# Kernel optimization log

Measured on AMD Instinct MI355X. Metric: run time of the kernel, lower is better.

Reference implementation:

```python
import jax, jax.numpy as jnp
import numpy as np

B, H, W, C = 8, 224, 224, 96
WS, SS, NH = 7, 3, 3  # window size, shift size, num heads
HD = C // NH
N = WS * WS
nW = (H // WS) * (W // WS)


def _rel_pos_index():
    coords = np.stack(np.meshgrid(np.arange(WS), np.arange(WS), indexing='ij'))  # (2,WS,WS)
    flat = coords.reshape(2, -1)
    rel = (flat[:, :, None] - flat[:, None, :]).transpose(1, 2, 0)  # (N,N,2)
    rel[:, :, 0] += WS - 1
    rel[:, :, 1] += WS - 1
    rel[:, :, 0] *= 2 * WS - 1
    return jnp.asarray(rel.sum(-1))  # (N,N) int


def _shift_mask():
    img = np.zeros((H, W), np.int32)
    cnt = 0
    sls = (slice(0, -WS), slice(-WS, -SS), slice(-SS, None))
    for hs in sls:
        for ws_ in sls:
            img[hs, ws_] = cnt
            cnt += 1
    m = img.reshape(H // WS, WS, W // WS, WS).transpose(0, 2, 1, 3).reshape(-1, N)  # (nW,N)
    diff = m[:, :, None] - m[:, None, :]
    return jnp.asarray(np.where(diff != 0, -100.0, 0.0).astype(np.float32))  # (nW,N,N)


def setup_inputs() -> dict:
    key = jax.random.key(0)
    ks = jax.random.split(key, 10)
    s = 0.02
    return {
        'x': jax.random.normal(ks[0], (B, H * W, C), jnp.float32),
        'mask': _shift_mask(),
        'norm1_g': jnp.ones((C,), jnp.float32),
        'norm1_b': jnp.zeros((C,), jnp.float32),
        'qkv_w': s * jax.random.normal(ks[1], (3 * C, C), jnp.float32),
        'qkv_b': jnp.zeros((3 * C,), jnp.float32),
        'rpb_table': s * jax.random.normal(ks[2], ((2 * WS - 1) * (2 * WS - 1), NH), jnp.float32),
        'proj_w': s * jax.random.normal(ks[3], (C, C), jnp.float32),
        'proj_b': jnp.zeros((C,), jnp.float32),
        'norm2_g': jnp.ones((C,), jnp.float32),
        'norm2_b': jnp.zeros((C,), jnp.float32),
        'fc1_w': s * jax.random.normal(ks[4], (4 * C, C), jnp.float32),
        'fc1_b': jnp.zeros((4 * C,), jnp.float32),
        'fc2_w': s * jax.random.normal(ks[5], (C, 4 * C), jnp.float32),
        'fc2_b': jnp.zeros((C,), jnp.float32),
    }


def _ln(x, g, b):
    mu = x.mean(-1, keepdims=True)
    var = x.var(-1, keepdims=True)
    return (x - mu) * jax.lax.rsqrt(var + 1e-5) * g + b


def _win_partition(x):  # (B,H,W,C) -> (B*nW, N, C)
    x = x.reshape(B, H // WS, WS, W // WS, WS, C)
    return x.transpose(0, 1, 3, 2, 4, 5).reshape(-1, N, C)


def _win_reverse(w):  # (B*nW, N, C) -> (B,H,W,C)
    w = w.reshape(B, H // WS, W // WS, WS, WS, C)
    return w.transpose(0, 1, 3, 2, 4, 5).reshape(B, H, W, C)


def reference(x, mask, norm1_g, norm1_b, qkv_w, qkv_b, rpb_table, proj_w, proj_b,
              norm2_g, norm2_b, fc1_w, fc1_b, fc2_w, fc2_b):
    rel_idx = _rel_pos_index()  # (N,N) constant
    shortcut = x
    h = _ln(x, norm1_g, norm1_b).reshape(B, H, W, C)
    h = jnp.roll(h, shift=(-SS, -SS), axis=(1, 2))  # cyclic shift
    xw = _win_partition(h)  # (B*nW, N, C)
    B_ = xw.shape[0]
    qkv = (xw @ qkv_w.T + qkv_b).reshape(B_, N, 3, NH, HD).transpose(2, 0, 3, 1, 4)
    q, k, v = qkv[0], qkv[1], qkv[2]  # (B_,NH,N,HD)
    scale = HD ** -0.5
    attn = jnp.einsum('bhid,bhjd->bhij', q * scale, k)  # (B_,NH,N,N)
    bias = rpb_table[rel_idx.reshape(-1)].reshape(N, N, NH).transpose(2, 0, 1)  # (NH,N,N)
    attn = attn + bias[None]
    attn = attn.reshape(B, nW, NH, N, N) + mask[None, :, None]
    attn = jax.nn.softmax(attn.reshape(B_, NH, N, N), axis=-1)
    out = jnp.einsum('bhij,bhjd->bhid', attn, v).transpose(0, 2, 1, 3).reshape(B_, N, C)
    out = out @ proj_w.T + proj_b
    h = _win_reverse(out)
    h = jnp.roll(h, shift=(SS, SS), axis=(1, 2)).reshape(B, H * W, C)
    x = shortcut + h
    # MLP
    m = _ln(x, norm2_g, norm2_b)
    m = jax.nn.gelu(m @ fc1_w.T + fc1_b, approximate=False)
    m = m @ fc2_w.T + fc2_b
    return x + m
```

## Files before the change

### kernel.cpp

```cpp
#include <hip/hip_runtime.h>
#include <hip/hip_bf16.h>
#include <stdint.h>

typedef __attribute__((ext_vector_type(4))) float f32x4;
typedef __bf16 bfv8 __attribute__((ext_vector_type(8)));
typedef unsigned short u16x8 __attribute__((ext_vector_type(8)));

#define DEV static __device__ __forceinline__

DEV float b2f(unsigned short h) {
    unsigned u = ((unsigned)h) << 16;
    return __builtin_bit_cast(float, u);
}
DEV unsigned short f2b(float f) {
    unsigned u = __builtin_bit_cast(unsigned, f);
    u += 0x7fffu + ((u >> 16) & 1u);
    return (unsigned short)(u >> 16);
}
DEV unsigned short f2bn(float f) {
    return __builtin_bit_cast(unsigned short, (__bf16)f);
}
DEV bfv8 ldb8(const unsigned short* p) {
    return __builtin_bit_cast(bfv8, *(const u16x8*)p);
}

static constexpr int T = 401408;

__global__ __launch_bounds__(256) void k_prep(const float* __restrict__ qkvw,
                                              const float* __restrict__ projw,
                                              const float* __restrict__ w1,
                                              const float* __restrict__ w2,
                                              const float* __restrict__ rpb,
                                              const float* __restrict__ mask,
                                              unsigned short* __restrict__ wb,
                                              float* __restrict__ cmb) {
    int i = blockIdx.x * 256 + threadIdx.x;
    if (i < 110592) {
        float v;
        if (i < 27648) v = qkvw[i];
        else if (i < 36864) v = projw[i - 27648];
        else if (i < 73728) v = w1[i - 36864];
        else v = w2[i - 73728];
        wb[i] = f2b(v);
    } else if (i < 110592 + 49152) {
        int j = i - 110592;
        int t = j / 12288, rem = j - t * 12288;
        int h = rem >> 12, nm = rem & 4095;
        int n = nm >> 6, m = nm & 63;
        float v = -10000.f;
        if (n < 49 && m < 49) {
            int i1 = n / 7, j1 = n - i1 * 7, i2 = m / 7, j2 = m - i2 * 7;
            int rel = (i1 - i2 + 6) * 13 + (j1 - j2 + 6);
            int rep = ((t & 1) ? 31 : 0) + ((t & 2) ? 992 : 0);
            v = rpb[rel * 3 + h] + mask[rep * 2401 + n * 49 + m];
        }
        cmb[j] = v;
    }
}

__global__ __launch_bounds__(192) void k_attnf(const float* __restrict__ x,
                                               const float* __restrict__ g1,
                                               const float* __restrict__ be1,
                                               const unsigned short* __restrict__ qkvwb,
                                               const float* __restrict__ qkvb,
                                               const float* __restrict__ cmb,
                                               unsigned short* __restrict__ aout) {
    __shared__ unsigned short smem[10368 + 3 * 5120];
    unsigned short* xs = smem;

    unsigned win = blockIdx.x;
    unsigned b = win >> 10, widx = win & 1023u;
    unsigned wi = widx >> 5, wj = widx & 31u;
    int tid = threadIdx.x, wv = tid >> 6, lane = tid & 63;
    int half = lane >> 5, lch = lane & 31;

    for (int it = 0; it < 9; ++it) {
        int tok = it * 6 + wv * 2 + half;
        if (tok < 49) {
            unsigned i = (unsigned)tok / 7u, j = (unsigned)tok - i * 7u;
            unsigned sr = wi * 7 + i + 3; if (sr >= 224) sr -= 224;
            unsigned sc = wj * 7 + j + 3; if (sc >= 224) sc -= 224;
            const float* src = x + (size_t)(b * 50176u + sr * 224u + sc) * 96;
            float v0 = src[lch], v1 = src[lch + 32], v2 = src[lch + 64];
            float s = v0 + v1 + v2, q = v0 * v0 + v1 * v1 + v2 * v2;
#pragma unroll
            for (int off = 1; off < 32; off <<= 1) {
                s += __shfl_xor(s, off);
                q += __shfl_xor(q, off);
            }
            float mu = s * (1.f / 96.f);
            float rstd = rsqrtf(q * (1.f / 96.f) - mu * mu + 1e-5f);
            xs[tok * 104 + lch]      = f2bn((v0 - mu) * rstd * g1[lch] + be1[lch]);
            xs[tok * 104 + lch + 32] = f2bn((v1 - mu) * rstd * g1[lch + 32] + be1[lch + 32]);
            xs[tok * 104 + lch + 64] = f2bn((v2 - mu) * rstd * g1[lch + 64] + be1[lch + 64]);
        }
    }
    for (int t = tid; t < 15 * 96; t += 192)
        xs[(49 + t / 96) * 104 + (t % 96)] = 0;
    __syncthreads();

    int h = wv;
    int rlo = lane & 15, g4 = lane >> 4;
    bfv8 a[4][3];
#pragma unroll
    for (int mt = 0; mt < 4; ++mt)
#pragma unroll
        for (int ks = 0; ks < 3; ++ks)
            a[mt][ks] = ldb8(xs + (mt * 16 + rlo) * 104 + ks * 32 + g4 * 8);
    __syncthreads();

    unsigned short* vtH = smem + h * 3456;
    unsigned short* qH  = smem + 10368 + h * 5120;
    unsigned short* kH  = qH + 2560;
    unsigned short* pH  = qH;

    const float SC = 0.17677669529663687f;
    int colbase[6] = {32 * h, 32 * h + 16, 96 + 32 * h, 96 + 32 * h + 16,
                      192 + 32 * h, 192 + 32 * h + 16};
#pragma unroll
    for (int grp = 0; grp < 2; ++grp) {
        bfv8 wS[3][3];
        float bS[3];
#pragma unroll
        for (int q3 = 0; q3 < 3; ++q3) {
            int c = colbase[grp * 3 + q3] + rlo;
            wS[q3][0] = ldb8(qkvwb + (size_t)c * 96 + g4 * 8);
            wS[q3][1] = ldb8(qkvwb + (size_t)c * 96 + 32 + g4 * 8);
            wS[q3][2] = ldb8(qkvwb + (size_t)c * 96 + 64 + g4 * 8);
            bS[q3] = qkvb[c];
        }
#pragma unroll
        for (int q3 = 0; q3 < 3; ++q3) {
            int nt = grp * 3 + q3;
#pragma unroll
            for (int mt = 0; mt < 4; ++mt) {
                f32x4 acc = {0.f, 0.f, 0.f, 0.f};
                acc = __builtin_amdgcn_mfma_f32_16x16x32_bf16(a[mt][0], wS[q3][0], acc, 0, 0, 0);
                acc = __builtin_amdgcn_mfma_f32_16x16x32_bf16(a[mt][1], wS[q3][1], acc, 0, 0, 0);
                acc = __builtin_amdgcn_mfma_f32_16x16x32_bf16(a[mt][2], wS[q3][2], acc, 0, 0, 0);
#pragma unroll
                for (int r = 0; r < 4; ++r) {
                    int row = mt * 16 + g4 * 4 + r;
                    float v = acc[r] + bS[q3];
                    if (nt < 2) qH[row * 40 + nt * 16 + rlo] = f2bn(v * SC);
                    else if (nt < 4) kH[row * 40 + (nt - 2) * 16 + rlo] = f2bn(v);
                    else vtH[((nt - 4) * 16 + rlo) * 72 + row] = f2bn(v);
                }
            }
        }
    }
    vtH[32 * 72 + lane] = 0x3F80;

    bfv8 qf[4], kf[4];
#pragma unroll
    for (int t = 0; t < 4; ++t) {
        qf[t] = ldb8(qH + (t * 16 + rlo) * 40 + g4 * 8);
        kf[t] = ldb8(kH + (t * 16 + rlo) * 40 + g4 * 8);
    }
    f32x4 s[4][4];
#pragma unroll
    for (int mt = 0; mt < 4; ++mt)
#pragma unroll
        for (int nt = 0; nt < 4; ++nt) {
            f32x4 acc0 = {0.f, 0.f, 0.f, 0.f};
            s[mt][nt] = __builtin_amdgcn_mfma_f32_16x16x32_bf16(qf[mt], kf[nt], acc0, 0, 0, 0);
        }
    int type = ((wi == 31) ? 2 : 0) | ((wj == 31) ? 1 : 0);
    const float* crow = cmb + ((size_t)(type * 3 + h) << 12);
#pragma unroll
    for (int mt = 0; mt < 4; ++mt) {
#pragma unroll
        for (int r = 0; r < 4; ++r) {
            int n = mt * 16 + g4 * 4 + r;
            const float* cr = crow + n * 64;
#pragma unroll
            for (int nt = 0; nt < 4; ++nt) {
                int m = nt * 16 + rlo;
                pH[n * 72 + m] = f2bn(__expf(s[mt][nt][r] + cr[m]));
            }
        }
    }
    bfv8 vf[2][3];
#pragma unroll
    for (int ks = 0; ks < 2; ++ks)
#pragma unroll
        for (int db = 0; db < 3; ++db)
            vf[ks][db] = ldb8(vtH + (db * 16 + rlo) * 72 + ks * 32 + g4 * 8);
#pragma unroll
    for (int mt = 0; mt < 4; ++mt) {
        bfv8 pa0 = ldb8(pH + (mt * 16 + rlo) * 72 + g4 * 8);
        bfv8 pa1 = ldb8(pH + (mt * 16 + rlo) * 72 + 32 + g4 * 8);
        f32x4 acc[3];
#pragma unroll
        for (int db = 0; db < 3; ++db) {
            acc[db] = {0.f, 0.f, 0.f, 0.f};
            acc[db] = __builtin_amdgcn_mfma_f32_16x16x32_bf16(pa0, vf[0][db], acc[db], 0, 0, 0);
            acc[db] = __builtin_amdgcn_mfma_f32_16x16x32_bf16(pa1, vf[1][db], acc[db], 0, 0, 0);
        }
        float inv[4];
#pragma unroll
        for (int r = 0; r < 4; ++r)
            inv[r] = 1.f / __shfl(acc[2][r], lane & 48);
#pragma unroll
        for (int db = 0; db < 2; ++db) {
#pragma unroll
            for (int r = 0; r < 4; ++r) {
                int n = mt * 16 + g4 * 4 + r;
                if (n < 49)
                    aout[((size_t)win * 49 + n) * 96 + h * 32 + db * 16 + rlo] =
                        f2bn(acc[db][r] * inv[r]);
            }
        }
    }
}

__global__ __launch_bounds__(256, 4) void k_pm(const unsigned short* __restrict__ aout,
                                               const unsigned short* __restrict__ projwb,
                                               const float* __restrict__ projb,
                                               const float* __restrict__ x,
                                               const float* __restrict__ g2,
                                               const float* __restrict__ be2,
                                               const unsigned short* __restrict__ w1b,
                                               const float* __restrict__ bias1,
                                               const unsigned short* __restrict__ w2b,
                                               const float* __restrict__ bias2,
                                               float* __restrict__ out) {
    __shared__ unsigned short smem[64 * 204];
    unsigned short* xn  = smem;
    unsigned short* m1t = smem;

    int lane = threadIdx.x & 63, wv = threadIdx.x >> 6;
    int rlo = lane & 15, g4 = lane >> 4;
    size_t tok0 = (size_t)blockIdx.x * 64;
    size_t rowW = tok0 + wv * 16;

    bfv8 a0[3];
    {
        const unsigned short* p = aout + (rowW + rlo) * 96 + g4 * 8;
        a0[0] = ldb8(p); a0[1] = ldb8(p + 32); a0[2] = ldb8(p + 64);
    }
    int pix[4];
#pragma unroll
    for (int r = 0; r < 4; ++r) {
        unsigned wt = (unsigned)(rowW + g4 * 4 + r);
        unsigned win = wt / 49u, n = wt - win * 49u;
        unsigned b = win >> 10, widx = win & 1023u;
        unsigned wi = widx >> 5, wj = widx & 31u;
        unsigned i = n / 7u, j = n - i * 7u;
        unsigned sr = wi * 7 + i + 3; if (sr >= 224) sr -= 224;
        unsigned sc = wj * 7 + j + 3; if (sc >= 224) sc -= 224;
        pix[r] = (int)(b * 50176u + sr * 224u + sc);
    }

    float xv[6][4];
    float rs_[4] = {0.f, 0.f, 0.f, 0.f}, rq_[4] = {0.f, 0.f, 0.f, 0.f};
    for (int nt = 0; nt < 6; ++nt) {
        int c = nt * 16 + rlo;
        bfv8 b0 = ldb8(projwb + (size_t)c * 96 + g4 * 8);
        bfv8 b1 = ldb8(projwb + (size_t)c * 96 + 32 + g4 * 8);
        bfv8 b2 = ldb8(projwb + (size_t)c * 96 + 64 + g4 * 8);
        float bv = projb[c];
        f32x4 acc = {0.f, 0.f, 0.f, 0.f};
        acc = __builtin_amdgcn_mfma_f32_16x16x32_bf16(a0[0], b0, acc, 0, 0, 0);
        acc = __builtin_amdgcn_mfma_f32_16x16x32_bf16(a0[1], b1, acc, 0, 0, 0);
        acc = __builtin_amdgcn_mfma_f32_16x16x32_bf16(a0[2], b2, acc, 0, 0, 0);
#pragma unroll
        for (int r = 0; r < 4; ++r) {
            float v = acc[r] + bv + x[(size_t)pix[r] * 96 + c];
            xv[nt][r] = v;
            rs_[r] += v;
            rq_[r] += v * v;
        }
    }
    float mu[4], rstd[4];
#pragma unroll
    for (int r = 0; r < 4; ++r) {
        float s = rs_[r], q = rq_[r];
#pragma unroll
        for (int off = 1; off < 16; off <<= 1) {
            s += __shfl_xor(s, off);
            q += __shfl_xor(q, off);
        }
        mu[r] = s * (1.f / 96.f);
        rstd[r] = rsqrtf(q * (1.f / 96.f) - mu[r] * mu[r] + 1e-5f);
    }
#pragma unroll
    for (int nt = 0; nt < 6; ++nt) {
        int c = nt * 16 + rlo;
        float gg = g2[c], bb = be2[c];
#pragma unroll
        for (int r = 0; r < 4; ++r) {
            int row = wv * 16 + g4 * 4 + r;
            xn[row * 104 + c] = f2bn((xv[nt][r] - mu[r]) * rstd[r] * gg + bb);
        }
    }
    __syncthreads();

    bfv8 a[4][3];
#pragma unroll
    for (int mt = 0; mt < 4; ++mt)
#pragma unroll
        for (int ks = 0; ks < 3; ++ks)
            a[mt][ks] = ldb8(xn + (mt * 16 + rlo) * 104 + ks * 32 + g4 * 8);
    __syncthreads();

    f32x4 acc2[6];
#pragma unroll
    for (int nt = 0; nt < 6; ++nt) acc2[nt] = {0.f, 0.f, 0.f, 0.f};

#pragma unroll
    for (int half = 0; half < 2; ++half) {
#pragma unroll
        for (int nt = 0; nt < 3; ++nt) {
            int cl = wv * 48 + nt * 16 + rlo;
            int c = half * 192 + cl;
            bfv8 b0 = ldb8(w1b + (size_t)c * 96 + g4 * 8);
            bfv8 b1 = ldb8(w1b + (size_t)c * 96 + 32 + g4 * 8);
            bfv8 b2 = ldb8(w1b + (size_t)c * 96 + 64 + g4 * 8);
            float bv = bias1[c];
#pragma unroll
            for (int mt = 0; mt < 4; ++mt) {
                f32x4 acc = {0.f, 0.f, 0.f, 0.f};
                acc = __builtin_amdgcn_mfma_f32_16x16x32_bf16(a[mt][0], b0, acc, 0, 0, 0);
                acc = __builtin_amdgcn_mfma_f32_16x16x32_bf16(a[mt][1], b1, acc, 0, 0, 0);
                acc = __builtin_amdgcn_mfma_f32_16x16x32_bf16(a[mt][2], b2, acc, 0, 0, 0);
#pragma unroll
                for (int r = 0; r < 4; ++r) {
                    float v = acc[r] + bv;
                    float z = 1.5957691216057308f * (v + 0.044715f * v * v * v);
                    v = v / (1.f + __expf(-z));
                    m1t[(mt * 16 + g4 * 4 + r) * 204 + cl] = f2bn(v);
                }
            }
        }
        __syncthreads();
#pragma unroll
        for (int ks = 0; ks < 6; ++ks) {
            bfv8 am = ldb8(m1t + (wv * 16 + rlo) * 204 + ks * 32 + g4 * 8);
#pragma unroll
            for (int nt = 0; nt < 6; ++nt) {
                bfv8 bw = ldb8(w2b + (size_t)(nt * 16 + rlo) * 384 + half * 192 + ks * 32 + g4 * 8);
                acc2[nt] = __builtin_amdgcn_mfma_f32_16x16x32_bf16(am, bw, acc2[nt], 0, 0, 0);
            }
        }
        if (half == 0) __syncthreads();
    }

#pragma unroll
    for (int nt = 0; nt < 6; ++nt) {
        int c = nt * 16 + rlo;
        float bv = bias2[c];
#pragma unroll
        for (int r = 0; r < 4; ++r)
            out[(size_t)pix[r] * 96 + c] = acc2[nt][r] + bv + xv[nt][r];
    }
}

extern "C" void kernel_launch(void* const* d_in, const int* in_sizes, int n_in,
                              void* d_out, int out_size, void* d_ws, size_t ws_size,
                              hipStream_t stream) {
    const float* x     = (const float*)d_in[0];
    const float* mask  = (const float*)d_in[1];
    const float* n1g   = (const float*)d_in[2];
    const float* n1b   = (const float*)d_in[3];
    const float* qkvw  = (const float*)d_in[4];
    const float* qkvb  = (const float*)d_in[5];
    const float* rpb   = (const float*)d_in[6];
    const float* projw = (const float*)d_in[7];
    const float* projb = (const float*)d_in[8];
    const float* n2g   = (const float*)d_in[9];
    const float* n2b   = (const float*)d_in[10];
    const float* fc1w  = (const float*)d_in[11];
    const float* fc1b  = (const float*)d_in[12];
    const float* fc2w  = (const float*)d_in[13];
    const float* fc2b  = (const float*)d_in[14];

    if (ws_size < 77488128ULL) return;
    char* ws = (char*)d_ws;
    unsigned short* aout = (unsigned short*)ws;
    unsigned short* wb   = (unsigned short*)(ws + 77070336);
    float*          cmb  = (float*)(ws + 77291520);
    float*          out  = (float*)d_out;

    unsigned short* qkvwb  = wb;
    unsigned short* projwb = wb + 27648;
    unsigned short* fc1wb  = wb + 36864;
    unsigned short* fc2wb  = wb + 73728;

    k_prep<<<624, 256, 0, stream>>>(qkvw, projw, fc1w, fc2w, rpb, mask, wb, cmb);
    k_attnf<<<8192, 192, 0, stream>>>(x, n1g, n1b, qkvwb, qkvb, cmb, aout);
    k_pm<<<T / 64, 256, 0, stream>>>(aout, projwb, projb, x, n2g, n2b,
                                     fc1wb, fc1b, fc2wb, fc2b, out);
}
```

Before: 566.7 us.

## Swap MFMA operand order to get transposed outputs enabling vectorized stores and loads

Every MFMA call now passes operands in swapped order, so each lane holds four consecutive output columns for one row instead of four rows for one column. This allows packed 4-wide bf16 shared/global stores, float4 loads of bias, mask, x and LayerNorm params, and it cuts the LayerNorm reduction from 4x4 shuffles to 2 shuffles per stat. The pixel index is computed once per lane rather than four times. k_pm launch bounds also drop from 4 to 3 blocks per SM, giving more registers but lower occupancy, and the V-transposed store remains scattered.

Result: faster. 520.4 us (-8.2%).

```diff
diff --git a/kernel.cpp b/kernel.cpp
--- a/kernel.cpp
+++ b/kernel.cpp
@@ -5,6 +5,7 @@
 typedef __attribute__((ext_vector_type(4))) float f32x4;
 typedef __bf16 bfv8 __attribute__((ext_vector_type(8)));
 typedef unsigned short u16x8 __attribute__((ext_vector_type(8)));
+typedef unsigned short u16x4 __attribute__((ext_vector_type(4)));
 
 #define DEV static __device__ __forceinline__
 
@@ -22,6 +23,11 @@
 }
 DEV bfv8 ldb8(const unsigned short* p) {
     return __builtin_bit_cast(bfv8, *(const u16x8*)p);
+}
+DEV void stb4(unsigned short* p, f32x4 v) {
+    u16x4 o;
+    o[0] = f2bn(v[0]); o[1] = f2bn(v[1]); o[2] = f2bn(v[2]); o[3] = f2bn(v[3]);
+    *(u16x4*)p = o;
 }
 
 static constexpr int T = 401408;
@@ -120,14 +126,14 @@
 #pragma unroll
     for (int grp = 0; grp < 2; ++grp) {
         bfv8 wS[3][3];
-        float bS[3];
+        f32x4 bS[3];
 #pragma unroll
         for (int q3 = 0; q3 < 3; ++q3) {
             int c = colbase[grp * 3 + q3] + rlo;
             wS[q3][0] = ldb8(qkvwb + (size_t)c * 96 + g4 * 8);
             wS[q3][1] = ldb8(qkvwb + (size_t)c * 96 + 32 + g4 * 8);
             wS[q3][2] = ldb8(qkvwb + (size_t)c * 96 + 64 + g4 * 8);
-            bS[q3] = qkvb[c];
+            bS[q3] = *(const f32x4*)(qkvb + colbase[grp * 3 + q3] + g4 * 4);
         }
 #pragma unroll
         for (int q3 = 0; q3 < 3; ++q3) {
@@ -135,16 +141,21 @@
 #pragma unroll
             for (int mt = 0; mt < 4; ++mt) {
                 f32x4 acc = {0.f, 0.f, 0.f, 0.f};
-                acc = __builtin_amdgcn_mfma_f32_16x16x32_bf16(a[mt][0], wS[q3][0], acc, 0, 0, 0);
-                acc = __builtin_amdgcn_mfma_f32_16x16x32_bf16(a[mt][1], wS[q3][1], acc, 0, 0, 0);
-                acc = __builtin_amdgcn_mfma_f32_16x16x32_bf16(a[mt][2], wS[q3][2], acc, 0, 0, 0);
-#pragma unroll
-                for (int r = 0; r < 4; ++r) {
-                    int row = mt * 16 + g4 * 4 + r;
-                    float v = acc[r] + bS[q3];
-                    if (nt < 2) qH[row * 40 + nt * 16 + rlo] = f2bn(v * SC);
-                    else if (nt < 4) kH[row * 40 + (nt - 2) * 16 + rlo] = f2bn(v);
-                    else vtH[((nt - 4) * 16 + rlo) * 72 + row] = f2bn(v);
+                acc = __builtin_amdgcn_mfma_f32_16x16x32_bf16(wS[q3][0], a[mt][0], acc, 0, 0, 0);
+                acc = __builtin_amdgcn_mfma_f32_16x16x32_bf16(wS[q3][1], a[mt][1], acc, 0, 0, 0);
+                acc = __builtin_amdgcn_mfma_f32_16x16x32_bf16(wS[q3][2], a[mt][2], acc, 0, 0, 0);
+                int token = mt * 16 + rlo;
+                if (nt < 2) {
+                    f32x4 v = (acc + bS[q3]) * SC;
+                    stb4(qH + token * 40 + nt * 16 + g4 * 4, v);
+                } else if (nt < 4) {
+                    f32x4 v = acc + bS[q3];
+                    stb4(kH + token * 40 + (nt - 2) * 16 + g4 * 4, v);
+                } else {
+#pragma unroll
+                    for (int r = 0; r < 4; ++r)
+                        vtH[((nt - 4) * 16 + g4 * 4 + r) * 72 + token] =
+                            f2bn(acc[r] + bS[q3][r]);
                 }
             }
         }
@@ -163,21 +174,21 @@
 #pragma unroll
         for (int nt = 0; nt < 4; ++nt) {
             f32x4 acc0 = {0.f, 0.f, 0.f, 0.f};
-            s[mt][nt] = __builtin_amdgcn_mfma_f32_16x16x32_bf16(qf[mt], kf[nt], acc0, 0, 0, 0);
+            s[mt][nt] = __builtin_amdgcn_mfma_f32_16x16x32_bf16(kf[nt], qf[mt], acc0, 0, 0, 0);
         }
     int type = ((wi == 31) ? 2 : 0) | ((wj == 31) ? 1 : 0);
     const float* crow = cmb + ((size_t)(type * 3 + h) << 12);
 #pragma unroll
     for (int mt = 0; mt < 4; ++mt) {
-#pragma unroll
-        for (int r = 0; r < 4; ++r) {
-            int n = mt * 16 + g4 * 4 + r;
-            const float* cr = crow + n * 64;
-#pragma unroll
-            for (int nt = 0; nt < 4; ++nt) {
-                int m = nt * 16 + rlo;
-                pH[n * 72 + m] = f2bn(__expf(s[mt][nt][r] + cr[m]));
-            }
+        int query = mt * 16 + rlo;
+        const float* cr = crow + query * 64;
+#pragma unroll
+        for (int nt = 0; nt < 4; ++nt) {
+            f32x4 cv = *(const f32x4*)(cr + nt * 16 + g4 * 4);
+            f32x4 p;
+#pragma unroll
+            for (int r = 0; r < 4; ++r) p[r] = __expf(s[mt][nt][r] + cv[r]);
+            stb4(pH + query * 72 + nt * 16 + g4 * 4, p);
         }
     }
     bfv8 vf[2][3];
@@ -194,27 +205,23 @@
 #pragma unroll
         for (int db = 0; db < 3; ++db) {
             acc[db] = {0.f, 0.f, 0.f, 0.f};
-            acc[db] = __builtin_amdgcn_mfma_f32_16x16x32_bf16(pa0, vf[0][db], acc[db], 0, 0, 0);
-            acc[db] = __builtin_amdgcn_mfma_f32_16x16x32_bf16(pa1, vf[1][db], acc[db], 0, 0, 0);
-        }
-        float inv[4];
-#pragma unroll
-        for (int r = 0; r < 4; ++r)
-            inv[r] = 1.f / __shfl(acc[2][r], lane & 48);
-#pragma unroll
-        for (int db = 0; db < 2; ++db) {
-#pragma unroll
-            for (int r = 0; r < 4; ++r) {
-                int n = mt * 16 + g4 * 4 + r;
-                if (n < 49)
-                    aout[((size_t)win * 49 + n) * 96 + h * 32 + db * 16 + rlo] =
-                        f2bn(acc[db][r] * inv[r]);
-            }
-        }
-    }
-}
-
-__global__ __launch_bounds__(256, 4) void k_pm(const unsigned short* __restrict__ aout,
+            acc[db] = __builtin_amdgcn_mfma_f32_16x16x32_bf16(vf[0][db], pa0, acc[db], 0, 0, 0);
+            acc[db] = __builtin_amdgcn_mfma_f32_16x16x32_bf16(vf[1][db], pa1, acc[db], 0, 0, 0);
+        }
+        float inv = 1.f / __shfl(acc[2][0], rlo);
+        int query = mt * 16 + rlo;
+        if (query < 49) {
+            unsigned short* ob = aout + ((size_t)win * 49 + query) * 96 + h * 32;
+#pragma unroll
+            for (int db = 0; db < 2; ++db) {
+                f32x4 v = acc[db] * inv;
+                stb4(ob + db * 16 + g4 * 4, v);
+            }
+        }
+    }
+}
+
+__global__ __launch_bounds__(256, 3) void k_pm(const unsigned short* __restrict__ aout,
                                                const unsigned short* __restrict__ projwb,
                                                const float* __restrict__ projb,
                                                const float* __restrict__ x,
@@ -239,60 +246,54 @@
         const unsigned short* p = aout + (rowW + rlo) * 96 + g4 * 8;
         a0[0] = ldb8(p); a0[1] = ldb8(p + 32); a0[2] = ldb8(p + 64);
     }
-    int pix[4];
-#pragma unroll
-    for (int r = 0; r < 4; ++r) {
-        unsigned wt = (unsigned)(rowW + g4 * 4 + r);
+    int pix;
+    {
+        unsigned wt = (unsigned)(rowW + rlo);
         unsigned win = wt / 49u, n = wt - win * 49u;
         unsigned b = win >> 10, widx = win & 1023u;
         unsigned wi = widx >> 5, wj = widx & 31u;
         unsigned i = n / 7u, j = n - i * 7u;
         unsigned sr = wi * 7 + i + 3; if (sr >= 224) sr -= 224;
         unsigned sc = wj * 7 + j + 3; if (sc >= 224) sc -= 224;
-        pix[r] = (int)(b * 50176u + sr * 224u + sc);
-    }
-
-    float xv[6][4];
-    float rs_[4] = {0.f, 0.f, 0.f, 0.f}, rq_[4] = {0.f, 0.f, 0.f, 0.f};
+        pix = (int)(b * 50176u + sr * 224u + sc);
+    }
+    f32x4 xr4[6];
+#pragma unroll
+    for (int nt = 0; nt < 6; ++nt)
+        xr4[nt] = *(const f32x4*)(x + (size_t)pix * 96 + nt * 16 + g4 * 4);
+
+    f32x4 xv[6];
+    float rs = 0.f, rq = 0.f;
     for (int nt = 0; nt < 6; ++nt) {
         int c = nt * 16 + rlo;
         bfv8 b0 = ldb8(projwb + (size_t)c * 96 + g4 * 8);
         bfv8 b1 = ldb8(projwb + (size_t)c * 96 + 32 + g4 * 8);
         bfv8 b2 = ldb8(projwb + (size_t)c * 96 + 64 + g4 * 8);
-        float bv = projb[c];
+        f32x4 bv = *(const f32x4*)(projb + nt * 16 + g4 * 4);
         f32x4 acc = {0.f, 0.f, 0.f, 0.f};
-        acc = __builtin_amdgcn_mfma_f32_16x16x32_bf16(a0[0], b0, acc, 0, 0, 0);
-        acc = __builtin_amdgcn_mfma_f32_16x16x32_bf16(a0[1], b1, acc, 0, 0, 0);
-        acc = __builtin_amdgcn_mfma_f32_16x16x32_bf16(a0[2], b2, acc, 0, 0, 0);
+        acc = __builtin_amdgcn_mfma_f32_16x16x32_bf16(b0, a0[0], acc, 0, 0, 0);
+        acc = __builtin_amdgcn_mfma_f32_16x16x32_bf16(b1, a0[1], acc, 0, 0, 0);
+        acc = __builtin_amdgcn_mfma_f32_16x16x32_bf16(b2, a0[2], acc, 0, 0, 0);
+        f32x4 v = acc + bv + xr4[nt];
+        xv[nt] = v;
 #pragma unroll
         for (int r = 0; r < 4; ++r) {
-            float v = acc[r] + bv + x[(size_t)pix[r] * 96 + c];
-            xv[nt][r] = v;
-            rs_[r] += v;
-            rq_[r] += v * v;
-        }
-    }
-    float mu[4], rstd[4];
-#pragma unroll
-    for (int r = 0; r < 4; ++r) {
-        float s = rs_[r], q = rq_[r];
-#pragma unroll
-        for (int off = 1; off < 16; off <<= 1) {
-            s += __shfl_xor(s, off);
-            q += __shfl_xor(q, off);
-        }
-        mu[r] = s * (1.f / 96.f);
-        rstd[r] = rsqrtf(q * (1.f / 96.f) - mu[r] * mu[r] + 1e-5f);
-    }
+            rs += v[r];
+            rq += v[r] * v[r];
+        }
+    }
+    rs += __shfl_xor(rs, 16); rq += __shfl_xor(rq, 16);
+    rs += __shfl_xor(rs, 32); rq += __shfl_xor(rq, 32);
+    float mu = rs * (1.f / 96.f);
+    float rstd = rsqrtf(rq * (1.f / 96.f) - mu * mu + 1e-5f);
 #pragma unroll
     for (int nt = 0; nt < 6; ++nt) {
-        int c = nt * 16 + rlo;
-        float gg = g2[c], bb = be2[c];
-#pragma unroll
-        for (int r = 0; r < 4; ++r) {
-            int row = wv * 16 + g4 * 4 + r;
-            xn[row * 104 + c] = f2bn((xv[nt][r] - mu[r]) * rstd[r] * gg + bb);
-        }
+        f32x4 gg = *(const f32x4*)(g2 + nt * 16 + g4 * 4);
+        f32x4 bb = *(const f32x4*)(be2 + nt * 16 + g4 * 4);
+        f32x4 v;
+#pragma unroll
+        for (int r = 0; r < 4; ++r) v[r] = (xv[nt][r] - mu) * rstd * gg[r] + bb[r];
+        stb4(xn + (wv * 16 + rlo) * 104 + nt * 16 + g4 * 4, v);
     }
     __syncthreads();
 
@@ -312,25 +313,26 @@
     for (int half = 0; half < 2; ++half) {
 #pragma unroll
         for (int nt = 0; nt < 3; ++nt) {
-            int cl = wv * 48 + nt * 16 + rlo;
-            int c = half * 192 + cl;
+            int cb = half * 192 + wv * 48 + nt * 16;
+            int c = cb + rlo;
             bfv8 b0 = ldb8(w1b + (size_t)c * 96 + g4 * 8);
             bfv8 b1 = ldb8(w1b + (size_t)c * 96 + 32 + g4 * 8);
             bfv8 b2 = ldb8(w1b + (size_t)c * 96 + 64 + g4 * 8);
-            float bv = bias1[c];
+            f32x4 bv = *(const f32x4*)(bias1 + cb + g4 * 4);
 #pragma unroll
             for (int mt = 0; mt < 4; ++mt) {
                 f32x4 acc = {0.f, 0.f, 0.f, 0.f};
-                acc = __builtin_amdgcn_mfma_f32_16x16x32_bf16(a[mt][0], b0, acc, 0, 0, 0);
-                acc = __builtin_amdgcn_mfma_f32_16x16x32_bf16(a[mt][1], b1, acc, 0, 0, 0);
-                acc = __builtin_amdgcn_mfma_f32_16x16x32_bf16(a[mt][2], b2, acc, 0, 0, 0);
+                acc = __builtin_amdgcn_mfma_f32_16x16x32_bf16(b0, a[mt][0], acc, 0, 0, 0);
+                acc = __builtin_amdgcn_mfma_f32_16x16x32_bf16(b1, a[mt][1], acc, 0, 0, 0);
+                acc = __builtin_amdgcn_mfma_f32_16x16x32_bf16(b2, a[mt][2], acc, 0, 0, 0);
+                f32x4 g;
 #pragma unroll
                 for (int r = 0; r < 4; ++r) {
-                    float v = acc[r] + bv;
+                    float v = acc[r] + bv[r];
                     float z = 1.5957691216057308f * (v + 0.044715f * v * v * v);
-                    v = v / (1.f + __expf(-z));
-                    m1t[(mt * 16 + g4 * 4 + r) * 204 + cl] = f2bn(v);
+                    g[r] = v / (1.f + __expf(-z));
                 }
+                stb4(m1t + (mt * 16 + rlo) * 204 + wv * 48 + nt * 16 + g4 * 4, g);
             }
         }
         __syncthreads();
@@ -340,7 +342,7 @@
 #pragma unroll
             for (int nt = 0; nt < 6; ++nt) {
                 bfv8 bw = ldb8(w2b + (size_t)(nt * 16 + rlo) * 384 + half * 192 + ks * 32 + g4 * 8);
-                acc2[nt] = __builtin_amdgcn_mfma_f32_16x16x32_bf16(am, bw, acc2[nt], 0, 0, 0);
+                acc2[nt] = __builtin_amdgcn_mfma_f32_16x16x32_bf16(bw, am, acc2[nt], 0, 0, 0);
             }
         }
         if (half == 0) __syncthreads();
@@ -348,11 +350,9 @@
 
 #pragma unroll
     for (int nt = 0; nt < 6; ++nt) {
-        int c = nt * 16 + rlo;
-        float bv = bias2[c];
-#pragma unroll
-        for (int r = 0; r < 4; ++r)
-            out[(size_t)pix[r] * 96 + c] = acc2[nt][r] + bv + xv[nt][r];
+        f32x4 bv = *(const f32x4*)(bias2 + nt * 16 + g4 * 4);
+        f32x4 ov = acc2[nt] + bv + xv[nt];
+        *(f32x4*)(out + (size_t)pix * 96 + nt * 16 + g4 * 4) = ov;
     }
 }
 
```
